# Kernel tuning notes

Hardware: AMD Instinct MI355X
Metric: run time of the kernel (lower is better)

Reference implementation:

```python
import jax, jax.numpy as jnp
import numpy as np

V = 50257   # vocab size (output_size / num_words)
H = 500     # hidden_size
S = 256     # source sequence length
MAXLEN = 64 # greedy decode steps
SOS = 1


def _gru_scan(xs, Wih, Whh, bih, bhh, reverse=False):
    """Run a GRU over xs: (S, Din) -> (outputs (S,H), final hidden (H,)).
    PyTorch gate order: r, z, n."""
    gx = xs @ Wih.T + bih  # (S, 3H), input-side gates precomputed
    Hh = Whh.shape[1]
    h0 = jnp.zeros((Hh,), dtype=xs.dtype)

    def step(h, g):
        gh = Whh @ h + bhh
        rx, zx, nx = jnp.split(g, 3)
        rh, zh, nh = jnp.split(gh, 3)
        r = jax.nn.sigmoid(rx + rh)
        z = jax.nn.sigmoid(zx + zh)
        n = jnp.tanh(nx + r * nh)
        h2 = (1.0 - z) * n + z * h
        return h2, h2

    hT, ys = jax.lax.scan(step, h0, gx, reverse=reverse)
    return ys, hT


def _gru_cell(x, h, Wih, Whh, bih, bhh):
    gx = Wih @ x + bih
    gh = Whh @ h + bhh
    rx, zx, nx = jnp.split(gx, 3)
    rh, zh, nh = jnp.split(gh, 3)
    r = jax.nn.sigmoid(rx + rh)
    z = jax.nn.sigmoid(zx + zh)
    n = jnp.tanh(nx + r * nh)
    return (1.0 - z) * n + z * h


def setup_inputs() -> dict:
    key = jax.random.key(0)
    ks = jax.random.split(key, 32)

    def p(k, shape):
        return jax.random.normal(k, shape, dtype=jnp.float32) * 0.05

    inp = {}
    inp["input_seq"] = jax.random.randint(ks[0], (S, 1), 0, V)
    inp["input_length"] = S
    inp["max_length"] = MAXLEN
    inp["emb"] = p(ks[1], (V, H))
    i = 2
    for name, din in [("enc0f", H), ("enc0b", H), ("enc1f", 2 * H), ("enc1b", 2 * H)]:
        inp[name + "_Wih"] = p(ks[i], (3 * H, din)); i += 1
        inp[name + "_Whh"] = p(ks[i], (3 * H, H)); i += 1
        inp[name + "_bih"] = p(ks[i], (3 * H,)); i += 1
        inp[name + "_bhh"] = p(ks[i], (3 * H,)); i += 1
    inp["dec_Wih"] = p(ks[i], (2, 3 * H, H)); i += 1
    inp["dec_Whh"] = p(ks[i], (2, 3 * H, H)); i += 1
    inp["dec_bih"] = p(ks[i], (2, 3 * H)); i += 1
    inp["dec_bhh"] = p(ks[i], (2, 3 * H)); i += 1
    inp["concat_W"] = p(ks[i], (H, 2 * H)); i += 1
    inp["concat_b"] = p(ks[i], (H,)); i += 1
    inp["out_W"] = p(ks[i], (V, H)); i += 1
    inp["out_b"] = p(ks[i], (V,)); i += 1
    return inp


def reference(input_seq, input_length, max_length, emb,
              enc0f_Wih, enc0f_Whh, enc0f_bih, enc0f_bhh,
              enc0b_Wih, enc0b_Whh, enc0b_bih, enc0b_bhh,
              enc1f_Wih, enc1f_Whh, enc1f_bih, enc1f_bhh,
              enc1b_Wih, enc1b_Whh, enc1b_bih, enc1b_bhh,
              dec_Wih, dec_Whh, dec_bih, dec_bhh,
              concat_W, concat_b, out_W, out_b):
    tokens = input_seq[:, 0]  # batch = 1
    ex = emb[tokens]          # (S, H) embedding lookup (dropout is eval no-op)

    # --- bidirectional 2-layer encoder GRU (full-length seq, batch=1) ---
    y0f, h0f = _gru_scan(ex, enc0f_Wih, enc0f_Whh, enc0f_bih, enc0f_bhh)
    y0b, h0b = _gru_scan(ex, enc0b_Wih, enc0b_Whh, enc0b_bih, enc0b_bhh, reverse=True)
    x1 = jnp.concatenate([y0f, y0b], axis=1)  # (S, 2H)
    y1f, _ = _gru_scan(x1, enc1f_Wih, enc1f_Whh, enc1f_bih, enc1f_bhh)
    y1b, _ = _gru_scan(x1, enc1b_Wih, enc1b_Whh, enc1b_bih, enc1b_bhh, reverse=True)
    enc_out = y1f + y1b  # (S, H): outputs[:, :H] + outputs[:, H:]

    # encoder_hidden[:n_layers] = [layer0_fwd, layer0_bwd] (PyTorch ordering)
    h_dec0 = jnp.stack([h0f, h0b])  # (2, H)

    def step(carry, _):
        h, tok = carry
        x = emb[tok]  # (H,)
        hs = []
        for l in range(2):  # 2 decoder GRU layers (dropout off in eval)
            hl = _gru_cell(x, h[l], dec_Wih[l], dec_Whh[l], dec_bih[l], dec_bhh[l])
            hs.append(hl)
            x = hl
        h2 = jnp.stack(hs)
        rnn = x  # (H,) top-layer output
        scores = enc_out @ rnn                 # dot attention: (S,)
        w = jax.nn.softmax(scores)
        ctx = w @ enc_out                      # (H,)
        c = jnp.tanh(concat_W @ jnp.concatenate([rnn, ctx]) + concat_b)
        probs = jax.nn.softmax(out_W @ c + out_b)  # (V,)
        tok2 = jnp.argmax(probs).astype(jnp.int32)
        return (h2, tok2), (tok2, probs)

    init = (h_dec0, jnp.asarray(SOS, dtype=jnp.int32))
    _, (all_tokens, all_probs) = jax.lax.scan(step, init, None, length=int(max_length))
    return all_tokens, all_probs
```

## Files before the change

### kernel.cpp

```cpp
#include <hip/hip_runtime.h>
#include <math.h>

typedef unsigned long long ull;

constexpr int H    = 500;
constexpr int H3   = 1500;
constexpr int SEQ  = 256;
constexpr int V    = 50257;
constexpr int TDEC = 64;
constexpr int NLT  = (V + 255) / 256;
constexpr int SB   = 50;
constexpr int UPB  = 10;
constexpr int NDB  = 256;
constexpr int VPB  = (V + NDB - 1) / NDB;

__device__ __forceinline__ float sigmoidf_(float x) { return 1.f / (1.f + expf(-x)); }

__device__ __forceinline__ float wred(float v) {
  #pragma unroll
  for (int off = 32; off > 0; off >>= 1) v += __shfl_down(v, off, 64);
  return v;
}

__device__ __forceinline__ float gload(const float* p) {
  return __hip_atomic_load((float*)p, __ATOMIC_RELAXED, __HIP_MEMORY_SCOPE_AGENT);
}
__device__ __forceinline__ void gstore(float* p, float v) {
  __hip_atomic_store(p, v, __ATOMIC_RELAXED, __HIP_MEMORY_SCOPE_AGENT);
}
__device__ __forceinline__ int gload_i(const int* p) {
  return __hip_atomic_load((int*)p, __ATOMIC_RELAXED, __HIP_MEMORY_SCOPE_AGENT);
}
__device__ __forceinline__ ull gload64(const ull* p) {
  return __hip_atomic_load((ull*)p, __ATOMIC_RELAXED, __HIP_MEMORY_SCOPE_AGENT);
}
__device__ __forceinline__ void gstore64(ull* p, ull v) {
  __hip_atomic_store(p, v, __ATOMIC_RELAXED, __HIP_MEMORY_SCOPE_AGENT);
}

template<int N>
__device__ __forceinline__ void poll_tags(const ull* tags, unsigned want,
                                          float* dst, int tid) {
  constexpr int NW = (N + 63) / 64;
  if (tid < 64) {
    ull v[NW];
    bool ok;
    do {
      ok = true;
      #pragma unroll
      for (int j = 0; j < NW; ++j) {
        int k = tid + (j << 6);
        if (k < N) {
          v[j] = gload64(&tags[k]);
          if ((unsigned)(v[j] >> 32) != want) ok = false;
        }
      }
      if (!ok) __builtin_amdgcn_s_sleep(1);
    } while (!ok);
    #pragma unroll
    for (int j = 0; j < NW; ++j) {
      int k = tid + (j << 6);
      if (k < N) dst[k] = __uint_as_float((unsigned)v[j]);
    }
  }
  __syncthreads();
}

__device__ __forceinline__ void poll2_tags(const ull* tA, float* dA,
                                           const ull* tB, float* dB,
                                           unsigned want, int tid) {
  if (tid < 64) {
    ull va[8], vb[4];
    bool ok;
    do {
      ok = true;
      #pragma unroll
      for (int j = 0; j < 8; ++j) {
        int k = tid + (j << 6);
        if (k < 500) {
          va[j] = gload64(&tA[k]);
          if ((unsigned)(va[j] >> 32) != want) ok = false;
        }
      }
      #pragma unroll
      for (int j = 0; j < 4; ++j) {
        int k = tid + (j << 6);
        vb[j] = gload64(&tB[k]);
        if ((unsigned)(vb[j] >> 32) != want) ok = false;
      }
      if (!ok) __builtin_amdgcn_s_sleep(1);
    } while (!ok);
    #pragma unroll
    for (int j = 0; j < 8; ++j) {
      int k = tid + (j << 6);
      if (k < 500) dA[k] = __uint_as_float((unsigned)va[j]);
    }
    #pragma unroll
    for (int j = 0; j < 4; ++j) {
      int k = tid + (j << 6);
      dB[k] = __uint_as_float((unsigned)vb[j]);
    }
  }
  __syncthreads();
}

__global__ void init_k(int* tok) {
  if (threadIdx.x == 0) tok[0] = 1;
}

__global__ void embed_k(const int* __restrict__ seq, const float* __restrict__ emb,
                        float* __restrict__ ex) {
  int t = blockIdx.x;
  int tok = seq[t];
  for (int i = threadIdx.x; i < H; i += blockDim.x)
    ex[(size_t)t * H + i] = emb[(size_t)tok * H + i];
}

__global__ __launch_bounds__(256) void gemm_nt(const float* __restrict__ X,
                                               const float* __restrict__ W,
                                               const float* __restrict__ bias,
                                               float* __restrict__ C,
                                               int M, int N, int K) {
  __shared__ float Xs[64][17];
  __shared__ float Ws[64][17];
  int bm = blockIdx.y * 64, bn = blockIdx.x * 64;
  int tid = threadIdx.x;
  int tx = tid % 16, ty = tid / 16;
  float acc[4][4] = {};
  for (int k0 = 0; k0 < K; k0 += 16) {
    for (int i = tid; i < 64 * 16; i += 256) {
      int m = i / 16, k = i % 16;
      int gm = bm + m, gk = k0 + k, gn = bn + m;
      Xs[m][k] = (gm < M && gk < K) ? X[(size_t)gm * K + gk] : 0.f;
      Ws[m][k] = (gn < N && gk < K) ? W[(size_t)gn * K + gk] : 0.f;
    }
    __syncthreads();
    #pragma unroll
    for (int k = 0; k < 16; ++k) {
      float xv[4], wv[4];
      #pragma unroll
      for (int i = 0; i < 4; ++i) xv[i] = Xs[ty * 4 + i][k];
      #pragma unroll
      for (int j = 0; j < 4; ++j) wv[j] = Ws[tx * 4 + j][k];
      #pragma unroll
      for (int i = 0; i < 4; ++i)
        #pragma unroll
        for (int j = 0; j < 4; ++j) acc[i][j] += xv[i] * wv[j];
    }
    __syncthreads();
  }
  for (int i = 0; i < 4; ++i) {
    int gm = bm + ty * 4 + i;
    if (gm >= M) continue;
    for (int j = 0; j < 4; ++j) {
      int gn = bn + tx * 4 + j;
      if (gn >= N) continue;
      C[(size_t)gm * N + gn] = acc[i][j] + bias[gn];
    }
  }
}

__global__ __launch_bounds__(512, 1) void gru_scan_tag(
    const float* __restrict__ gxF, const float* __restrict__ gxB,
    const float* __restrict__ WhhF, const float* __restrict__ WhhB,
    const float* __restrict__ bhhF, const float* __restrict__ bhhB,
    ull* __restrict__ tAF, ull* __restrict__ tBF,
    ull* __restrict__ tAB, ull* __restrict__ tBB,
    float* __restrict__ yF, float* __restrict__ yB, int ystride) {
  __shared__ float w_lds[30 * 500];
  __shared__ float gates[32];
  __shared__ float h_lds[512];
  int dir = blockIdx.x / SB;
  int bu  = blockIdx.x % SB;
  int u0  = bu * UPB;
  const float* gx  = dir ? gxB : gxF;
  const float* Whh = dir ? WhhB : WhhF;
  const float* bhh = dir ? bhhB : bhhF;
  ull* tagA = dir ? tAB : tAF;
  ull* tagB = dir ? tBB : tBF;
  float* y  = dir ? yB : yF;
  int tid = threadIdx.x, lane = tid & 63, wid = tid >> 6;

  for (int idx = tid; idx < 30 * 500; idx += 512) {
    int r = idx / 500, k = idx - r * 500;
    int g = r / UPB, lu = r - g * UPB;
    w_lds[idx] = Whh[(size_t)(g * 500 + u0 + lu) * 500 + k];
  }
  int u = u0 + tid;
  float br = 0.f, bz = 0.f, bn = 0.f;
  if (tid < UPB) { br = bhh[u]; bz = bhh[500 + u]; bn = bhh[1000 + u]; }
  h_lds[tid] = 0.f;
  __syncthreads();

  for (int t = 0; t < SEQ; ++t) {
    ull* wout = (t & 1) ? tagA : tagB;
    ull* win  = (t & 1) ? tagB : tagA;
    int teff = dir ? (SEQ - 1 - t) : t;

    float gxr = 0.f, gxz = 0.f, gxn = 0.f;
    if (tid < UPB) {
      const float* g = gx + (size_t)teff * H3;
      gxr = g[u]; gxz = g[500 + u]; gxn = g[1000 + u];
    }

    if (t > 0 && wid == 0) {
      ull v[8];
      for (;;) {
        bool ok = true;
        #pragma unroll
        for (int j = 0; j < 8; ++j) {
          int k = lane + 64 * j;
          if (k < 500) {
            v[j] = gload64(&win[k]);
            if ((unsigned)(v[j] >> 32) != (unsigned)t) ok = false;
          }
        }
        if (ok) break;
        __builtin_amdgcn_s_sleep(1);
      }
      #pragma unroll
      for (int j = 0; j < 8; ++j) {
        int k = lane + 64 * j;
        if (k < 500) h_lds[k] = __uint_as_float((unsigned)v[j]);
      }
    }
    __syncthreads();

    float hreg[8];
    #pragma unroll
    for (int j = 0; j < 8; ++j) {
      int k = lane + 64 * j;
      hreg[j] = (k < 500) ? h_lds[k] : 0.f;
    }
    for (int r = wid; r < 30; r += 8) {
      const float* wr = &w_lds[r * 500];
      float acc = 0.f;
      #pragma unroll
      for (int j = 0; j < 8; ++j) {
        int k = lane + 64 * j;
        if (k < 500) acc += wr[k] * hreg[j];
      }
      acc = wred(acc);
      if (lane == 0) gates[r] = acc;
    }
    __syncthreads();
    if (tid < UPB) {
      float hold = h_lds[u];
      float rr = sigmoidf_(gxr + gates[tid]           + br);
      float zz = sigmoidf_(gxz + gates[UPB + tid]     + bz);
      float nn = tanhf(    gxn + rr * (gates[2 * UPB + tid] + bn));
      float hp = (1.f - zz) * nn + zz * hold;
      ull pv = ((ull)(unsigned)(t + 1) << 32) | (ull)__float_as_uint(hp);
      gstore64(&wout[u], pv);
      y[(size_t)teff * ystride + u] = hp;
    }
  }
}

__global__ void unpack_k(const ull* __restrict__ ta, const ull* __restrict__ tb,
                         float* __restrict__ ha, float* __restrict__ hb_) {
  int i = threadIdx.x;
  if (i < 500) {
    ha[i]  = __uint_as_float((unsigned)ta[i]);
    hb_[i] = __uint_as_float((unsigned)tb[i]);
  }
}

__global__ void add_k(const float* __restrict__ a, const float* __restrict__ b,
                      float* __restrict__ c, int n) {
  int i = blockIdx.x * blockDim.x + threadIdx.x;
  if (i < n) c[i] = a[i] + b[i];
}

__device__ __forceinline__ void cell_unit_pub(int u, int lane,
    const float* xf, const float* hf,
    const float* __restrict__ Wih, const float* __restrict__ Whh,
    const float* __restrict__ bih, const float* __restrict__ bhh,
    float* hplain, ull* htag, unsigned want) {
  float g[6];
  #pragma unroll
  for (int kind = 0; kind < 6; ++kind) {
    const float* row = (kind < 3) ? (Wih + (size_t)(kind * 500 + u) * 500)
                                  : (Whh + (size_t)((kind - 3) * 500 + u) * 500);
    const float* vec = (kind < 3) ? xf : hf;
    float acc = 0.f;
    #pragma unroll
    for (int j = 0; j < 8; ++j) {
      int k = lane + 64 * j;
      if (k < 500) acc += row[k] * vec[k];
    }
    g[kind] = wred(acc);
  }
  if (lane == 0) {
    float r = sigmoidf_(g[0] + bih[u]        + g[3] + bhh[u]);
    float z = sigmoidf_(g[1] + bih[500 + u]  + g[4] + bhh[500 + u]);
    float n = tanhf(    g[2] + bih[1000 + u] + r * (g[5] + bhh[1000 + u]));
    float hv = (1.f - z) * n + z * hf[u];
    hplain[u] = hv;
    gstore64(&htag[u], ((ull)want << 32) | (ull)__float_as_uint(hv));
  }
}

__global__ __launch_bounds__(512, 1) void dec_step_v5(
    int* __restrict__ tokp, const float* __restrict__ emb,
    const float* __restrict__ h0in, float* __restrict__ h0out,
    const float* __restrict__ h1in, float* __restrict__ h1out,
    const float* __restrict__ dWih, const float* __restrict__ dWhh,
    const float* __restrict__ dbih, const float* __restrict__ dbhh,
    const float* __restrict__ enc_out, const float* __restrict__ cW,
    const float* __restrict__ cb,
    const float* __restrict__ outW, const float* __restrict__ outb,
    ull* __restrict__ th0, ull* __restrict__ th1, ull* __restrict__ tsc,
    ull* __restrict__ tctx, ull* __restrict__ tcvec,
    float* __restrict__ lg_w, const float* __restrict__ lg_r,
    float* __restrict__ pm, float* __restrict__ ps, int* __restrict__ pix,
    float* __restrict__ stats, float* __restrict__ out_tokens,
    float* __restrict__ out_probs, int* __restrict__ dcnt, int st) {
  __shared__ float4 v4[250];
  __shared__ float hfull[512];
  __shared__ float red[256], sc[256];
  __shared__ float wm[8], wsum[8]; __shared__ int wix[8];
  __shared__ float mm[256], ms[256]; __shared__ int mi[256];
  __shared__ int lastf;
  float* xf = (float*)v4;
  float* hf = xf + 500;
  int tid = threadIdx.x, lane = tid & 63, wid = tid >> 6, blk = blockIdx.x;
  unsigned want = (unsigned)(st + 1);
  bool worker = blk < 63;
  int u = blk * 8 + wid;

  if (!worker && st > 0) {
    float mM = stats[2 * (st - 1)], iS = stats[2 * (st - 1) + 1];
    int base = blk * VPB;
    for (int r = tid; r < VPB; r += 512) {
      int v = base + r;
      if (v < V) out_probs[(size_t)(st - 1) * V + v] = expf(lg_r[v] - mM) * iS;
    }
  }

  if (worker) {
    int tk = tokp[0];
    for (int i = tid; i < 500; i += 512) {
      xf[i] = emb[(size_t)tk * 500 + i];
      hf[i] = h0in[i];
    }
    __syncthreads();
    if (u < 500) cell_unit_pub(u, lane, xf, hf, dWih, dWhh, dbih, dbhh,
                               h0out, th0, want);
    __syncthreads();

    if (tid >= 64) for (int i = tid - 64; i < 500; i += 448) hf[i] = h1in[i];
    poll_tags<500>(th0, want, xf, tid);
    if (u < 500) cell_unit_pub(u, lane, xf, hf,
        dWih + 750000, dWhh + 750000, dbih + 1500, dbhh + 1500,
        h1out, th1, want);
    __syncthreads();

    if (blk < 32) {
      poll_tags<500>(th1, want, hfull, tid);
      int s = blk * 8 + wid;
      const float* row = enc_out + (size_t)s * 500;
      float acc = 0.f;
      #pragma unroll
      for (int j = 0; j < 8; ++j) {
        int k = lane + 64 * j;
        if (k < 500) acc += row[k] * hfull[k];
      }
      acc = wred(acc);
      if (lane == 0)
        gstore64(&tsc[s], ((ull)want << 32) | (ull)__float_as_uint(acc));
      poll_tags<256>(tsc, want, sc, tid);
    } else {
      poll2_tags(th1, hfull, tsc, sc, want, tid);
    }

    {
      float myv = (tid < 256) ? sc[tid] : 0.f;
      if (tid < 256) red[tid] = myv;
      __syncthreads();
      for (int s = 128; s > 0; s >>= 1) {
        if (tid < s) red[tid] = fmaxf(red[tid], red[tid + s]);
        __syncthreads();
      }
      float m = red[0]; __syncthreads();
      float e = 0.f;
      if (tid < 256) { e = expf(myv - m); red[tid] = e; }
      __syncthreads();
      for (int s = 128; s > 0; s >>= 1) {
        if (tid < s) red[tid] += red[tid + s];
        __syncthreads();
      }
      float inv = 1.f / red[0]; __syncthreads();
      if (tid < 256) sc[tid] = e * inv;
      __syncthreads();
      int j = blk * 8 + wid;
      if (j < 500) {
        float acc = 0.f;
        #pragma unroll
        for (int q = 0; q < 4; ++q) {
          int s = lane + 64 * q;
          acc += sc[s] * enc_out[(size_t)s * 500 + j];
        }
        acc = wred(acc);
        if (lane == 0)
          gstore64(&tctx[j], ((ull)want << 32) | (ull)__float_as_uint(acc));
      }
    }

    if (tid >= 64) for (int i = tid - 64; i < 500; i += 448) xf[i] = hfull[i];
    poll_tags<500>(tctx, want, hf, tid);
    {
      int i = blk * 8 + wid;
      if (i < 500) {
        const float* row = cW + (size_t)i * 1000;
        float acc = 0.f;
        #pragma unroll
        for (int j = 0; j < 16; ++j) {
          int k = lane + 64 * j;
          if (k < 1000) acc += row[k] * xf[k];
        }
        acc = wred(acc);
        if (lane == 0) {
          float cv = tanhf(acc + cb[i]);
          gstore64(&tcvec[i], ((ull)want << 32) | (ull)__float_as_uint(cv));
        }
      }
    }
    __syncthreads();
  }

  poll_tags<500>(tcvec, want, xf, tid);
  const float4* c4 = v4;
  {
    int lstart = wid * 25, lend = (wid + 1) * 25; if (lend > VPB) lend = VPB;
    int r0 = blk * VPB + lstart, r1 = blk * VPB + lend; if (r1 > V) r1 = V;
    float m = -1e30f, ssum = 0.f; int ix = V;
    for (int rb = r0; rb < r1; rb += 4) {
      int nr = r1 - rb; if (nr > 4) nr = 4;
      float a[4] = {0.f, 0.f, 0.f, 0.f};
      #pragma unroll
      for (int q = 0; q < 2; ++q) {
        int k4 = lane + 64 * q;
        if (k4 < 125) {
          float4 cc = c4[k4];
          #pragma unroll
          for (int rr = 0; rr < 4; ++rr) {
            if (rr < nr) {
              float4 w4 = ((const float4*)(outW + (size_t)(rb + rr) * 500))[k4];
              a[rr] += w4.x * cc.x + w4.y * cc.y + w4.z * cc.z + w4.w * cc.w;
            }
          }
        }
      }
      #pragma unroll
      for (int rr = 0; rr < 4; ++rr) {
        if (rr < nr) {
          float l = wred(a[rr]);
          if (lane == 0) {
            l += outb[rb + rr];
            lg_w[rb + rr] = l;
            if (l > m) { ssum = ssum * expf(m - l) + 1.f; m = l; ix = rb + rr; }
            else       { ssum += expf(l - m); }
          }
        }
      }
    }
    if (lane == 0) { wm[wid] = m; wsum[wid] = ssum; wix[wid] = ix; }
  }
  __syncthreads();
  if (tid == 0) {
    float M = wm[0], S = wsum[0]; int I = wix[0];
    for (int w = 1; w < 8; ++w) {
      if (wm[w] > M) { S = S * expf(M - wm[w]) + wsum[w]; M = wm[w]; I = wix[w]; }
      else           { S += wsum[w] * expf(wm[w] - M); }
    }
    gstore(&pm[blk], M); gstore(&ps[blk], S);
    __hip_atomic_store(&pix[blk], I, __ATOMIC_RELAXED, __HIP_MEMORY_SCOPE_AGENT);
    __builtin_amdgcn_s_waitcnt(0);
    int prev = __hip_atomic_fetch_add(&dcnt[st], 1, __ATOMIC_RELAXED,
                                      __HIP_MEMORY_SCOPE_AGENT);
    lastf = (prev == NDB - 1) ? 1 : 0;
  }
  __syncthreads();

  if (lastf) {
    if (tid < 256) { mm[tid] = gload(&pm[tid]); ms[tid] = gload(&ps[tid]); mi[tid] = gload_i(&pix[tid]); }
    __syncthreads();
    for (int s = 128; s > 0; s >>= 1) {
      if (tid < s) {
        float ma = mm[tid], mb = mm[tid + s];
        float sa = ms[tid], sb = ms[tid + s];
        int ia = mi[tid], ib = mi[tid + s];
        if (mb > ma || (mb == ma && ib < ia)) {
          ms[tid] = sa * expf(ma - mb) + sb; mm[tid] = mb; mi[tid] = ib;
        } else {
          ms[tid] = sa + sb * expf(mb - ma);
        }
      }
      __syncthreads();
    }
    if (tid == 0) {
      tokp[0] = mi[0];
      out_tokens[st] = (float)mi[0];
      stats[2 * st] = mm[0];
      stats[2 * st + 1] = 1.f / ms[0];
    }
  }

  if (worker && st > 0) {
    float mM = stats[2 * (st - 1)], iS = stats[2 * (st - 1) + 1];
    int base = blk * VPB;
    for (int r = tid; r < VPB; r += 512) {
      int v = base + r;
      if (v < V) out_probs[(size_t)(st - 1) * V + v] = expf(lg_r[v] - mM) * iS;
    }
  }
}

__global__ __launch_bounds__(256) void probs_k(const float* __restrict__ logits,
    const float* __restrict__ stats, float* __restrict__ out_probs) {
  int v = blockIdx.x * 256 + threadIdx.x;
  if (v < V) out_probs[v] = expf(logits[v] - stats[0]) * stats[1];
}

extern "C" void kernel_launch(void* const* d_in, const int* in_sizes, int n_in,
                              void* d_out, int out_size, void* d_ws, size_t ws_size,
                              hipStream_t stream) {
  const int*   seq   = (const int*)d_in[0];
  const float* emb   = (const float*)d_in[3];
  const float* e0f_Wih = (const float*)d_in[4];
  const float* e0f_Whh = (const float*)d_in[5];
  const float* e0f_bih = (const float*)d_in[6];
  const float* e0f_bhh = (const float*)d_in[7];
  const float* e0b_Wih = (const float*)d_in[8];
  const float* e0b_Whh = (const float*)d_in[9];
  const float* e0b_bih = (const float*)d_in[10];
  const float* e0b_bhh = (const float*)d_in[11];
  const float* e1f_Wih = (const float*)d_in[12];
  const float* e1f_Whh = (const float*)d_in[13];
  const float* e1f_bih = (const float*)d_in[14];
  const float* e1f_bhh = (const float*)d_in[15];
  const float* e1b_Wih = (const float*)d_in[16];
  const float* e1b_Whh = (const float*)d_in[17];
  const float* e1b_bih = (const float*)d_in[18];
  const float* e1b_bhh = (const float*)d_in[19];
  const float* dWih = (const float*)d_in[20];
  const float* dWhh = (const float*)d_in[21];
  const float* dbih = (const float*)d_in[22];
  const float* dbhh = (const float*)d_in[23];
  const float* cW   = (const float*)d_in[24];
  const float* cb   = (const float*)d_in[25];
  const float* outW = (const float*)d_in[26];
  const float* outb = (const float*)d_in[27];

  float* w = (float*)d_ws;
  float* ex      = w;
  float* x1      = ex + 128000;
  float* gxf     = x1 + 256000;
  float* gxb     = gxf + 384000;
  float* y1f     = gxb + 384000;
  float* y1b     = y1f + 128000;
  float* enc_out = y1b + 128000;
  float* hL0FA   = enc_out + 128000;
  float* hL0BA   = hL0FA + 512;
  float* dsc0    = hL0BA + 512;
  float* dsc1    = dsc0 + 512;
  float* lg0     = dsc1 + 512;
  float* lg1     = lg0 + 50432;
  float* pm      = lg1 + 50432;
  float* ps      = pm + 256;
  float* stats   = ps + 256;
  int*   pix     = (int*)(stats + 192);
  int*   tokp    = pix + 256;
  int*   dcnt    = tokp + 64;
  ull*   htag    = (ull*)(dcnt + 64);
  ull* tL0F_A = htag;        ull* tL0F_B = htag + 512;
  ull* tL0B_A = htag + 1024; ull* tL0B_B = htag + 1536;
  ull* tL1F_A = htag + 2048; ull* tL1F_B = htag + 2560;
  ull* tL1B_A = htag + 3072; ull* tL1B_B = htag + 3584;
  ull*   dtag    = htag + 4096;
  ull* th0   = dtag;        ull* th1  = dtag + 512;
  ull* tsc   = dtag + 1024; ull* tctx = dtag + 1280;
  ull* tcvec = dtag + 1792;

  float* outf = (float*)d_out;

  hipMemsetAsync(dcnt, 0, 64 * sizeof(int) + 6400 * sizeof(ull), stream);

  init_k<<<1, 64, 0, stream>>>(tokp);
  embed_k<<<SEQ, 128, 0, stream>>>(seq, emb, ex);

  gemm_nt<<<dim3(24, 4), 256, 0, stream>>>(ex, e0f_Wih, e0f_bih, gxf, SEQ, H3, H);
  gemm_nt<<<dim3(24, 4), 256, 0, stream>>>(ex, e0b_Wih, e0b_bih, gxb, SEQ, H3, H);
  gru_scan_tag<<<2 * SB, 512, 0, stream>>>(gxf, gxb, e0f_Whh, e0b_Whh,
      e0f_bhh, e0b_bhh, tL0F_A, tL0F_B, tL0B_A, tL0B_B, x1, x1 + 500, 1000);
  unpack_k<<<1, 512, 0, stream>>>(tL0F_A, tL0B_A, hL0FA, hL0BA);

  gemm_nt<<<dim3(24, 4), 256, 0, stream>>>(x1, e1f_Wih, e1f_bih, gxf, SEQ, H3, 2 * H);
  gemm_nt<<<dim3(24, 4), 256, 0, stream>>>(x1, e1b_Wih, e1b_bih, gxb, SEQ, H3, 2 * H);
  gru_scan_tag<<<2 * SB, 512, 0, stream>>>(gxf, gxb, e1f_Whh, e1b_Whh,
      e1f_bhh, e1b_bhh, tL1F_A, tL1F_B, tL1B_A, tL1B_B, y1f, y1b, 500);
  add_k<<<(SEQ * H + 255) / 256, 256, 0, stream>>>(y1f, y1b, enc_out, SEQ * H);

  float* h0c = hL0FA; float* h0a = dsc0;
  float* h1c = hL0BA; float* h1a = dsc1;
  for (int st = 0; st < TDEC; ++st) {
    float* lg_w = (st & 1) ? lg1 : lg0;
    float* lg_r = (st & 1) ? lg0 : lg1;
    dec_step_v5<<<NDB, 512, 0, stream>>>(tokp, emb, h0c, h0a, h1c, h1a,
        dWih, dWhh, dbih, dbhh, enc_out, cW, cb, outW, outb,
        th0, th1, tsc, tctx, tcvec, lg_w, lg_r,
        pm, ps, pix, stats, outf, outf + TDEC, dcnt, st);
    float* t0 = h0c; h0c = h0a; h0a = t0;
    float* t1 = h1c; h1c = h1a; h1a = t1;
  }
  probs_k<<<NLT, 256, 0, stream>>>(((TDEC - 1) & 1) ? lg1 : lg0,
      stats + 2 * (TDEC - 1), outf + TDEC + (size_t)(TDEC - 1) * V);
}
```

Measured before the change: 6.294 ms.

## Fuse decoder steps into one persistent kernel and keep encoder Whh in registers

Replaces the 64 per-step decoder kernel launches with one persistent kernel. Steps are chained through tagged global flags: the token is published as a tagged 64-bit word and the hidden states are double-buffered as tag arrays. Separately, the encoder GRU scan now holds each warp's Whh rows in registers instead of LDS, which removes LDS reads from the recurrent matvec but raises register pressure. The aim is to cut launch overhead and kernel boundaries between steps. The cost is spin-polling across all 256 blocks, which depends on every block being co-resident.

After: 6.212 ms. No clear change (-1.3%).

```diff
diff --git a/kernel.cpp b/kernel.cpp
--- a/kernel.cpp
+++ b/kernel.cpp
@@ -104,8 +104,8 @@
   __syncthreads();
 }
 
-__global__ void init_k(int* tok) {
-  if (threadIdx.x == 0) tok[0] = 1;
+__global__ void init_k(ull* ttok) {
+  if (threadIdx.x == 0) ttok[0] = (1ull << 32) | 1ull;
 }
 
 __global__ void embed_k(const int* __restrict__ seq, const float* __restrict__ emb,
@@ -167,7 +167,6 @@
     ull* __restrict__ tAF, ull* __restrict__ tBF,
     ull* __restrict__ tAB, ull* __restrict__ tBB,
     float* __restrict__ yF, float* __restrict__ yB, int ystride) {
-  __shared__ float w_lds[30 * 500];
   __shared__ float gates[32];
   __shared__ float h_lds[512];
   int dir = blockIdx.x / SB;
@@ -181,10 +180,16 @@
   float* y  = dir ? yB : yF;
   int tid = threadIdx.x, lane = tid & 63, wid = tid >> 6;
 
-  for (int idx = tid; idx < 30 * 500; idx += 512) {
-    int r = idx / 500, k = idx - r * 500;
-    int g = r / UPB, lu = r - g * UPB;
-    w_lds[idx] = Whh[(size_t)(g * 500 + u0 + lu) * 500 + k];
+  float wreg[4][8];
+  #pragma unroll
+  for (int rr = 0; rr < 4; ++rr) {
+    int r = wid + 8 * rr;
+    #pragma unroll
+    for (int j = 0; j < 8; ++j) {
+      int k = lane + 64 * j;
+      wreg[rr][j] = (r < 30 && k < 500)
+          ? Whh[(size_t)((r / UPB) * 500 + u0 + (r % UPB)) * 500 + k] : 0.f;
+    }
   }
   int u = u0 + tid;
   float br = 0.f, bz = 0.f, bn = 0.f;
@@ -232,16 +237,16 @@
       int k = lane + 64 * j;
       hreg[j] = (k < 500) ? h_lds[k] : 0.f;
     }
-    for (int r = wid; r < 30; r += 8) {
-      const float* wr = &w_lds[r * 500];
-      float acc = 0.f;
-      #pragma unroll
-      for (int j = 0; j < 8; ++j) {
-        int k = lane + 64 * j;
-        if (k < 500) acc += wr[k] * hreg[j];
-      }
-      acc = wred(acc);
-      if (lane == 0) gates[r] = acc;
+    #pragma unroll
+    for (int rr = 0; rr < 4; ++rr) {
+      int r = wid + 8 * rr;
+      if (r < 30) {
+        float acc = 0.f;
+        #pragma unroll
+        for (int j = 0; j < 8; ++j) acc += wreg[rr][j] * hreg[j];
+        acc = wred(acc);
+        if (lane == 0) gates[r] = acc;
+      }
     }
     __syncthreads();
     if (tid < UPB) {
@@ -254,15 +259,16 @@
       gstore64(&wout[u], pv);
       y[(size_t)teff * ystride + u] = hp;
     }
-  }
-}
-
-__global__ void unpack_k(const ull* __restrict__ ta, const ull* __restrict__ tb,
-                         float* __restrict__ ha, float* __restrict__ hb_) {
+    __syncthreads();
+  }
+}
+
+__global__ void seed_k(const ull* __restrict__ tf, const ull* __restrict__ tb,
+                       ull* __restrict__ th0a, ull* __restrict__ th1a) {
   int i = threadIdx.x;
   if (i < 500) {
-    ha[i]  = __uint_as_float((unsigned)ta[i]);
-    hb_[i] = __uint_as_float((unsigned)tb[i]);
+    th0a[i] = (ull)(unsigned)tf[i];
+    th1a[i] = (ull)(unsigned)tb[i];
   }
 }
 
@@ -272,11 +278,11 @@
   if (i < n) c[i] = a[i] + b[i];
 }
 
-__device__ __forceinline__ void cell_unit_pub(int u, int lane,
+__device__ __forceinline__ void cell_unit_tag(int u, int lane,
     const float* xf, const float* hf,
     const float* __restrict__ Wih, const float* __restrict__ Whh,
     const float* __restrict__ bih, const float* __restrict__ bhh,
-    float* hplain, ull* htag, unsigned want) {
+    ull* htag, unsigned want) {
   float g[6];
   #pragma unroll
   for (int kind = 0; kind < 6; ++kind) {
@@ -296,224 +302,237 @@
     float z = sigmoidf_(g[1] + bih[500 + u]  + g[4] + bhh[500 + u]);
     float n = tanhf(    g[2] + bih[1000 + u] + r * (g[5] + bhh[1000 + u]));
     float hv = (1.f - z) * n + z * hf[u];
-    hplain[u] = hv;
     gstore64(&htag[u], ((ull)want << 32) | (ull)__float_as_uint(hv));
   }
 }
 
-__global__ __launch_bounds__(512, 1) void dec_step_v5(
-    int* __restrict__ tokp, const float* __restrict__ emb,
-    const float* __restrict__ h0in, float* __restrict__ h0out,
-    const float* __restrict__ h1in, float* __restrict__ h1out,
+__global__ __launch_bounds__(512, 1) void dec_persist(
+    const float* __restrict__ emb,
     const float* __restrict__ dWih, const float* __restrict__ dWhh,
     const float* __restrict__ dbih, const float* __restrict__ dbhh,
     const float* __restrict__ enc_out, const float* __restrict__ cW,
     const float* __restrict__ cb,
     const float* __restrict__ outW, const float* __restrict__ outb,
-    ull* __restrict__ th0, ull* __restrict__ th1, ull* __restrict__ tsc,
-    ull* __restrict__ tctx, ull* __restrict__ tcvec,
-    float* __restrict__ lg_w, const float* __restrict__ lg_r,
+    ull* __restrict__ th0a, ull* __restrict__ th0b,
+    ull* __restrict__ th1a, ull* __restrict__ th1b,
+    ull* __restrict__ tsc, ull* __restrict__ tctx, ull* __restrict__ tcvec,
+    ull* __restrict__ ttok,
+    float* __restrict__ lg0, float* __restrict__ lg1,
     float* __restrict__ pm, float* __restrict__ ps, int* __restrict__ pix,
     float* __restrict__ stats, float* __restrict__ out_tokens,
-    float* __restrict__ out_probs, int* __restrict__ dcnt, int st) {
+    float* __restrict__ out_probs, int* __restrict__ dcnt) {
   __shared__ float4 v4[250];
   __shared__ float hfull[512];
   __shared__ float red[256], sc[256];
   __shared__ float wm[8], wsum[8]; __shared__ int wix[8];
   __shared__ float mm[256], ms[256]; __shared__ int mi[256];
-  __shared__ int lastf;
+  __shared__ int lastf, sh_tk;
   float* xf = (float*)v4;
   float* hf = xf + 500;
   int tid = threadIdx.x, lane = tid & 63, wid = tid >> 6, blk = blockIdx.x;
-  unsigned want = (unsigned)(st + 1);
   bool worker = blk < 63;
   int u = blk * 8 + wid;
 
-  if (!worker && st > 0) {
-    float mM = stats[2 * (st - 1)], iS = stats[2 * (st - 1) + 1];
-    int base = blk * VPB;
-    for (int r = tid; r < VPB; r += 512) {
-      int v = base + r;
-      if (v < V) out_probs[(size_t)(st - 1) * V + v] = expf(lg_r[v] - mM) * iS;
-    }
-  }
-
-  if (worker) {
-    int tk = tokp[0];
-    for (int i = tid; i < 500; i += 512) {
-      xf[i] = emb[(size_t)tk * 500 + i];
-      hf[i] = h0in[i];
-    }
-    __syncthreads();
-    if (u < 500) cell_unit_pub(u, lane, xf, hf, dWih, dWhh, dbih, dbhh,
-                               h0out, th0, want);
-    __syncthreads();
-
-    if (tid >= 64) for (int i = tid - 64; i < 500; i += 448) hf[i] = h1in[i];
-    poll_tags<500>(th0, want, xf, tid);
-    if (u < 500) cell_unit_pub(u, lane, xf, hf,
-        dWih + 750000, dWhh + 750000, dbih + 1500, dbhh + 1500,
-        h1out, th1, want);
-    __syncthreads();
-
-    if (blk < 32) {
-      poll_tags<500>(th1, want, hfull, tid);
-      int s = blk * 8 + wid;
-      const float* row = enc_out + (size_t)s * 500;
-      float acc = 0.f;
-      #pragma unroll
-      for (int j = 0; j < 8; ++j) {
-        int k = lane + 64 * j;
-        if (k < 500) acc += row[k] * hfull[k];
-      }
-      acc = wred(acc);
-      if (lane == 0)
-        gstore64(&tsc[s], ((ull)want << 32) | (ull)__float_as_uint(acc));
-      poll_tags<256>(tsc, want, sc, tid);
-    } else {
-      poll2_tags(th1, hfull, tsc, sc, want, tid);
-    }
-
+  for (int st = 0; st < TDEC; ++st) {
+    unsigned want = (unsigned)(st + 1);
+    ull* h0r = (st & 1) ? th0b : th0a;
+    ull* h0w = (st & 1) ? th0a : th0b;
+    ull* h1r = (st & 1) ? th1b : th1a;
+    ull* h1w = (st & 1) ? th1a : th1b;
+    float* lg_w = (st & 1) ? lg1 : lg0;
+    const float* lg_r = (st & 1) ? lg0 : lg1;
+
+    if (worker) {
+      if (tid == 0) {
+        ull tv;
+        for (;;) {
+          tv = gload64(ttok);
+          if ((unsigned)(tv >> 32) == want) break;
+          __builtin_amdgcn_s_sleep(1);
+        }
+        sh_tk = (int)(unsigned)tv;
+      }
+      __syncthreads();
+      int tk = sh_tk;
+      if (tid >= 64) {
+        for (int i = tid - 64; i < 500; i += 448) xf[i] = emb[(size_t)tk * 500 + i];
+      } else {
+        #pragma unroll
+        for (int j = 0; j < 8; ++j) {
+          int k = tid + (j << 6);
+          if (k < 500) hf[k] = __uint_as_float((unsigned)gload64(&h0r[k]));
+        }
+      }
+      __syncthreads();
+      if (u < 500) cell_unit_tag(u, lane, xf, hf, dWih, dWhh, dbih, dbhh, h0w, want);
+      __syncthreads();
+
+      if (tid >= 64) {
+        for (int i = tid - 64; i < 500; i += 448)
+          hf[i] = __uint_as_float((unsigned)gload64(&h1r[i]));
+      }
+      poll_tags<500>(h0w, want, xf, tid);
+      if (u < 500) cell_unit_tag(u, lane, xf, hf,
+          dWih + 750000, dWhh + 750000, dbih + 1500, dbhh + 1500, h1w, want);
+      __syncthreads();
+
+      if (blk < 32) {
+        poll_tags<500>(h1w, want, hfull, tid);
+        int s = blk * 8 + wid;
+        const float* row = enc_out + (size_t)s * 500;
+        float acc = 0.f;
+        #pragma unroll
+        for (int j = 0; j < 8; ++j) {
+          int k = lane + 64 * j;
+          if (k < 500) acc += row[k] * hfull[k];
+        }
+        acc = wred(acc);
+        if (lane == 0) gstore64(&tsc[s], ((ull)want << 32) | (ull)__float_as_uint(acc));
+        poll_tags<256>(tsc, want, sc, tid);
+      } else {
+        poll2_tags(h1w, hfull, tsc, sc, want, tid);
+      }
+
+      {
+        float myv = (tid < 256) ? sc[tid] : 0.f;
+        if (tid < 256) red[tid] = myv;
+        __syncthreads();
+        for (int s = 128; s > 0; s >>= 1) {
+          if (tid < s) red[tid] = fmaxf(red[tid], red[tid + s]);
+          __syncthreads();
+        }
+        float m = red[0]; __syncthreads();
+        float e = 0.f;
+        if (tid < 256) { e = expf(myv - m); red[tid] = e; }
+        __syncthreads();
+        for (int s = 128; s > 0; s >>= 1) {
+          if (tid < s) red[tid] += red[tid + s];
+          __syncthreads();
+        }
+        float inv = 1.f / red[0]; __syncthreads();
+        if (tid < 256) sc[tid] = e * inv;
+        __syncthreads();
+        int j = blk * 8 + wid;
+        if (j < 500) {
+          float acc = 0.f;
+          #pragma unroll
+          for (int q = 0; q < 4; ++q) {
+            int s = lane + 64 * q;
+            acc += sc[s] * enc_out[(size_t)s * 500 + j];
+          }
+          acc = wred(acc);
+          if (lane == 0) gstore64(&tctx[j], ((ull)want << 32) | (ull)__float_as_uint(acc));
+        }
+      }
+
+      if (tid >= 64) for (int i = tid - 64; i < 500; i += 448) xf[i] = hfull[i];
+      poll_tags<500>(tctx, want, hf, tid);
+      {
+        int i = blk * 8 + wid;
+        if (i < 500) {
+          const float* row = cW + (size_t)i * 1000;
+          float acc = 0.f;
+          #pragma unroll
+          for (int j = 0; j < 16; ++j) {
+            int k = lane + 64 * j;
+            if (k < 1000) acc += row[k] * xf[k];
+          }
+          acc = wred(acc);
+          if (lane == 0)
+            gstore64(&tcvec[i], ((ull)want << 32) | (ull)__float_as_uint(tanhf(acc + cb[i])));
+        }
+      }
+      __syncthreads();
+    }
+
+    poll_tags<500>(tcvec, want, xf, tid);
+    const float4* c4 = v4;
     {
-      float myv = (tid < 256) ? sc[tid] : 0.f;
-      if (tid < 256) red[tid] = myv;
+      int lstart = wid * 25, lend = (wid + 1) * 25; if (lend > VPB) lend = VPB;
+      int r0 = blk * VPB + lstart, r1 = blk * VPB + lend; if (r1 > V) r1 = V;
+      float m = -1e30f, ssum = 0.f; int ix = V;
+      for (int rb = r0; rb < r1; rb += 4) {
+        int nr = r1 - rb; if (nr > 4) nr = 4;
+        float a[4] = {0.f, 0.f, 0.f, 0.f};
+        #pragma unroll
+        for (int q = 0; q < 2; ++q) {
+          int k4 = lane + 64 * q;
+          if (k4 < 125) {
+            float4 cc = c4[k4];
+            #pragma unroll
+            for (int rr = 0; rr < 4; ++rr) {
+              if (rr < nr) {
+                float4 w4 = ((const float4*)(outW + (size_t)(rb + rr) * 500))[k4];
+                a[rr] += w4.x * cc.x + w4.y * cc.y + w4.z * cc.z + w4.w * cc.w;
+              }
+            }
+          }
+        }
+        #pragma unroll
+        for (int rr = 0; rr < 4; ++rr) {
+          if (rr < nr) {
+            float l = wred(a[rr]);
+            if (lane == 0) {
+              l += outb[rb + rr];
+              lg_w[rb + rr] = l;
+              if (l > m) { ssum = ssum * expf(m - l) + 1.f; m = l; ix = rb + rr; }
+              else       { ssum += expf(l - m); }
+            }
+          }
+        }
+      }
+      if (lane == 0) { wm[wid] = m; wsum[wid] = ssum; wix[wid] = ix; }
+    }
+    __syncthreads();
+    if (tid == 0) {
+      float M = wm[0], S = wsum[0]; int I = wix[0];
+      for (int w2 = 1; w2 < 8; ++w2) {
+        if (wm[w2] > M) { S = S * expf(M - wm[w2]) + wsum[w2]; M = wm[w2]; I = wix[w2]; }
+        else            { S += wsum[w2] * expf(wm[w2] - M); }
+      }
+      gstore(&pm[blk], M); gstore(&ps[blk], S);
+      __hip_atomic_store(&pix[blk], I, __ATOMIC_RELAXED, __HIP_MEMORY_SCOPE_AGENT);
+      __builtin_amdgcn_s_waitcnt(0);
+      int prev = __hip_atomic_fetch_add(&dcnt[st], 1, __ATOMIC_RELAXED,
+                                        __HIP_MEMORY_SCOPE_AGENT);
+      lastf = (prev == NDB - 1) ? 1 : 0;
+    }
+    __syncthreads();
+
+    if (lastf) {
+      if (tid < 256) { mm[tid] = gload(&pm[tid]); ms[tid] = gload(&ps[tid]); mi[tid] = gload_i(&pix[tid]); }
       __syncthreads();
       for (int s = 128; s > 0; s >>= 1) {
-        if (tid < s) red[tid] = fmaxf(red[tid], red[tid + s]);
+        if (tid < s) {
+          float ma = mm[tid], mb = mm[tid + s];
+          float sa = ms[tid], sb = ms[tid + s];
+          int ia = mi[tid], ib = mi[tid + s];
+          if (mb > ma || (mb == ma && ib < ia)) {
+            ms[tid] = sa * expf(ma - mb) + sb; mm[tid] = mb; mi[tid] = ib;
+          } else {
+            ms[tid] = sa + sb * expf(mb - ma);
+          }
+        }
         __syncthreads();
       }
-      float m = red[0]; __syncthreads();
-      float e = 0.f;
-      if (tid < 256) { e = expf(myv - m); red[tid] = e; }
-      __syncthreads();
-      for (int s = 128; s > 0; s >>= 1) {
-        if (tid < s) red[tid] += red[tid + s];
-        __syncthreads();
-      }
-      float inv = 1.f / red[0]; __syncthreads();
-      if (tid < 256) sc[tid] = e * inv;
-      __syncthreads();
-      int j = blk * 8 + wid;
-      if (j < 500) {
-        float acc = 0.f;
-        #pragma unroll
-        for (int q = 0; q < 4; ++q) {
-          int s = lane + 64 * q;
-          acc += sc[s] * enc_out[(size_t)s * 500 + j];
-        }
-        acc = wred(acc);
-        if (lane == 0)
-          gstore64(&tctx[j], ((ull)want << 32) | (ull)__float_as_uint(acc));
-      }
-    }
-
-    if (tid >= 64) for (int i = tid - 64; i < 500; i += 448) xf[i] = hfull[i];
-    poll_tags<500>(tctx, want, hf, tid);
-    {
-      int i = blk * 8 + wid;
-      if (i < 500) {
-        const float* row = cW + (size_t)i * 1000;
-        float acc = 0.f;
-        #pragma unroll
-        for (int j = 0; j < 16; ++j) {
-          int k = lane + 64 * j;
-          if (k < 1000) acc += row[k] * xf[k];
-        }
-        acc = wred(acc);
-        if (lane == 0) {
-          float cv = tanhf(acc + cb[i]);
-          gstore64(&tcvec[i], ((ull)want << 32) | (ull)__float_as_uint(cv));
-        }
-      }
-    }
-    __syncthreads();
-  }
-
-  poll_tags<500>(tcvec, want, xf, tid);
-  const float4* c4 = v4;
-  {
-    int lstart = wid * 25, lend = (wid + 1) * 25; if (lend > VPB) lend = VPB;
-    int r0 = blk * VPB + lstart, r1 = blk * VPB + lend; if (r1 > V) r1 = V;
-    float m = -1e30f, ssum = 0.f; int ix = V;
-    for (int rb = r0; rb < r1; rb += 4) {
-      int nr = r1 - rb; if (nr > 4) nr = 4;
-      float a[4] = {0.f, 0.f, 0.f, 0.f};
-      #pragma unroll
-      for (int q = 0; q < 2; ++q) {
-        int k4 = lane + 64 * q;
-        if (k4 < 125) {
-          float4 cc = c4[k4];
-          #pragma unroll
-          for (int rr = 0; rr < 4; ++rr) {
-            if (rr < nr) {
-              float4 w4 = ((const float4*)(outW + (size_t)(rb + rr) * 500))[k4];
-              a[rr] += w4.x * cc.x + w4.y * cc.y + w4.z * cc.z + w4.w * cc.w;
-            }
-          }
-        }
-      }
-      #pragma unroll
-      for (int rr = 0; rr < 4; ++rr) {
-        if (rr < nr) {
-          float l = wred(a[rr]);
-          if (lane == 0) {
-            l += outb[rb + rr];
-            lg_w[rb + rr] = l;
-            if (l > m) { ssum = ssum * expf(m - l) + 1.f; m = l; ix = rb + rr; }
-            else       { ssum += expf(l - m); }
-          }
-        }
-      }
-    }
-    if (lane == 0) { wm[wid] = m; wsum[wid] = ssum; wix[wid] = ix; }
-  }
-  __syncthreads();
-  if (tid == 0) {
-    float M = wm[0], S = wsum[0]; int I = wix[0];
-    for (int w = 1; w < 8; ++w) {
-      if (wm[w] > M) { S = S * expf(M - wm[w]) + wsum[w]; M = wm[w]; I = wix[w]; }
-      else           { S += wsum[w] * expf(wm[w] - M); }
-    }
-    gstore(&pm[blk], M); gstore(&ps[blk], S);
-    __hip_atomic_store(&pix[blk], I, __ATOMIC_RELAXED, __HIP_MEMORY_SCOPE_AGENT);
-    __builtin_amdgcn_s_waitcnt(0);
-    int prev = __hip_atomic_fetch_add(&dcnt[st], 1, __ATOMIC_RELAXED,
-                                      __HIP_MEMORY_SCOPE_AGENT);
-    lastf = (prev == NDB - 1) ? 1 : 0;
-  }
-  __syncthreads();
-
-  if (lastf) {
-    if (tid < 256) { mm[tid] = gload(&pm[tid]); ms[tid] = gload(&ps[tid]); mi[tid] = gload_i(&pix[tid]); }
-    __syncthreads();
-    for (int s = 128; s > 0; s >>= 1) {
-      if (tid < s) {
-        float ma = mm[tid], mb = mm[tid + s];
-        float sa = ms[tid], sb = ms[tid + s];
-        int ia = mi[tid], ib = mi[tid + s];
-        if (mb > ma || (mb == ma && ib < ia)) {
-          ms[tid] = sa * expf(ma - mb) + sb; mm[tid] = mb; mi[tid] = ib;
-        } else {
-          ms[tid] = sa + sb * expf(mb - ma);
-        }
-      }
-      __syncthreads();
-    }
-    if (tid == 0) {
-      tokp[0] = mi[0];
-      out_tokens[st] = (float)mi[0];
-      stats[2 * st] = mm[0];
-      stats[2 * st + 1] = 1.f / ms[0];
-    }
-  }
-
-  if (worker && st > 0) {
-    float mM = stats[2 * (st - 1)], iS = stats[2 * (st - 1) + 1];
-    int base = blk * VPB;
-    for (int r = tid; r < VPB; r += 512) {
-      int v = base + r;
-      if (v < V) out_probs[(size_t)(st - 1) * V + v] = expf(lg_r[v] - mM) * iS;
-    }
+      if (tid == 0) {
+        out_tokens[st] = (float)mi[0];
+        gstore(&stats[2 * st], mm[0]);
+        gstore(&stats[2 * st + 1], 1.f / ms[0]);
+        __builtin_amdgcn_s_waitcnt(0);
+        gstore64(ttok, ((ull)(unsigned)(st + 2) << 32) | (ull)(unsigned)mi[0]);
+      }
+    }
+
+    if (st > 0) {
+      float mM = gload(&stats[2 * (st - 1)]), iS = gload(&stats[2 * (st - 1) + 1]);
+      int base = blk * VPB;
+      for (int r = tid; r < VPB; r += 512) {
+        int v = base + r;
+        if (v < V) out_probs[(size_t)(st - 1) * V + v] = expf(lg_r[v] - mM) * iS;
+      }
+    }
+    __syncthreads();
   }
 }
 
@@ -561,40 +580,35 @@
   float* y1f     = gxb + 384000;
   float* y1b     = y1f + 128000;
   float* enc_out = y1b + 128000;
-  float* hL0FA   = enc_out + 128000;
-  float* hL0BA   = hL0FA + 512;
-  float* dsc0    = hL0BA + 512;
-  float* dsc1    = dsc0 + 512;
-  float* lg0     = dsc1 + 512;
+  float* lg0     = enc_out + 128000;
   float* lg1     = lg0 + 50432;
   float* pm      = lg1 + 50432;
   float* ps      = pm + 256;
   float* stats   = ps + 256;
   int*   pix     = (int*)(stats + 192);
-  int*   tokp    = pix + 256;
-  int*   dcnt    = tokp + 64;
+  int*   dcnt    = pix + 256;
   ull*   htag    = (ull*)(dcnt + 64);
   ull* tL0F_A = htag;        ull* tL0F_B = htag + 512;
   ull* tL0B_A = htag + 1024; ull* tL0B_B = htag + 1536;
   ull* tL1F_A = htag + 2048; ull* tL1F_B = htag + 2560;
   ull* tL1B_A = htag + 3072; ull* tL1B_B = htag + 3584;
   ull*   dtag    = htag + 4096;
-  ull* th0   = dtag;        ull* th1  = dtag + 512;
-  ull* tsc   = dtag + 1024; ull* tctx = dtag + 1280;
-  ull* tcvec = dtag + 1792;
+  ull* th0a  = dtag;        ull* th0b = dtag + 512;
+  ull* th1a  = dtag + 1024; ull* th1b = dtag + 1536;
+  ull* tsc   = dtag + 2048; ull* tctx = dtag + 2304;
+  ull* tcvec = dtag + 2816; ull* ttok = dtag + 3328;
 
   float* outf = (float*)d_out;
 
-  hipMemsetAsync(dcnt, 0, 64 * sizeof(int) + 6400 * sizeof(ull), stream);
-
-  init_k<<<1, 64, 0, stream>>>(tokp);
+  hipMemsetAsync(dcnt, 0, 64 * sizeof(int) + 7488 * sizeof(ull), stream);
+
+  init_k<<<1, 64, 0, stream>>>(ttok);
   embed_k<<<SEQ, 128, 0, stream>>>(seq, emb, ex);
 
   gemm_nt<<<dim3(24, 4), 256, 0, stream>>>(ex, e0f_Wih, e0f_bih, gxf, SEQ, H3, H);
   gemm_nt<<<dim3(24, 4), 256, 0, stream>>>(ex, e0b_Wih, e0b_bih, gxb, SEQ, H3, H);
   gru_scan_tag<<<2 * SB, 512, 0, stream>>>(gxf, gxb, e0f_Whh, e0b_Whh,
       e0f_bhh, e0b_bhh, tL0F_A, tL0F_B, tL0B_A, tL0B_B, x1, x1 + 500, 1000);
-  unpack_k<<<1, 512, 0, stream>>>(tL0F_A, tL0B_A, hL0FA, hL0BA);
 
   gemm_nt<<<dim3(24, 4), 256, 0, stream>>>(x1, e1f_Wih, e1f_bih, gxf, SEQ, H3, 2 * H);
   gemm_nt<<<dim3(24, 4), 256, 0, stream>>>(x1, e1b_Wih, e1b_bih, gxb, SEQ, H3, 2 * H);
@@ -602,18 +616,13 @@
       e1f_bhh, e1b_bhh, tL1F_A, tL1F_B, tL1B_A, tL1B_B, y1f, y1b, 500);
   add_k<<<(SEQ * H + 255) / 256, 256, 0, stream>>>(y1f, y1b, enc_out, SEQ * H);
 
-  float* h0c = hL0FA; float* h0a = dsc0;
-  float* h1c = hL0BA; float* h1a = dsc1;
-  for (int st = 0; st < TDEC; ++st) {
-    float* lg_w = (st & 1) ? lg1 : lg0;
-    float* lg_r = (st & 1) ? lg0 : lg1;
-    dec_step_v5<<<NDB, 512, 0, stream>>>(tokp, emb, h0c, h0a, h1c, h1a,
-        dWih, dWhh, dbih, dbhh, enc_out, cW, cb, outW, outb,
-        th0, th1, tsc, tctx, tcvec, lg_w, lg_r,
-        pm, ps, pix, stats, outf, outf + TDEC, dcnt, st);
-    float* t0 = h0c; h0c = h0a; h0a = t0;
-    float* t1 = h1c; h1c = h1a; h1a = t1;
-  }
+  seed_k<<<1, 512, 0, stream>>>(tL0F_A, tL0B_A, th0a, th1a);
+
+  dec_persist<<<NDB, 512, 0, stream>>>(emb,
+      dWih, dWhh, dbih, dbhh, enc_out, cW, cb, outW, outb,
+      th0a, th0b, th1a, th1b, tsc, tctx, tcvec, ttok,
+      lg0, lg1, pm, ps, pix, stats, outf, outf + TDEC, dcnt);
+
   probs_k<<<NLT, 256, 0, stream>>>(((TDEC - 1) & 1) ? lg1 : lg0,
       stats + 2 * (TDEC - 1), outf + TDEC + (size_t)(TDEC - 1) * V);
 }
```
